# Kernel tuning notes

Measured on AMD Instinct MI355X. Metric: run time of the kernel, lower is better.

Reference implementation:

```python
import jax, jax.numpy as jnp
import numpy as np

N = 100000      # nodes
R = 8           # relations
E_DIM = 128     # embedding dim
N_EDGES = 1600000  # n * avg_degree(16)


def setup_inputs() -> dict:
    key = jax.random.key(0)
    k1, k2, k3, k4, k5 = jax.random.split(key, 5)
    x = jax.random.normal(k1, (N, E_DIM), dtype=jnp.float32)
    # xavier-ish scale for (r, e, e) relation weights
    weights = jax.random.normal(k2, (R, E_DIM, E_DIM), dtype=jnp.float32) * (1.0 / np.sqrt(E_DIM))
    edge_rel = jax.random.randint(k3, (N_EDGES,), 0, R, dtype=jnp.int32)
    edge_src = jax.random.randint(k4, (N_EDGES,), 0, N, dtype=jnp.int32)
    edge_dst = jax.random.randint(k5, (N_EDGES,), 0, N, dtype=jnp.int32)
    return dict(x=x, weights=weights, edge_rel=edge_rel, edge_src=edge_src, edge_dst=edge_dst)


def reference(x, weights, edge_rel, edge_src, edge_dst):
    n, e = x.shape
    r = weights.shape[0]
    # sparse adjacency row index: relation-block row = rel * n + dst  (shape rn)
    rows = edge_rel.astype(jnp.int32) * n + edge_dst.astype(jnp.int32)
    # row-normalized values: vals = 1 / row_degree (util.sum_sparse)
    deg = jax.ops.segment_sum(jnp.ones(rows.shape, dtype=x.dtype), rows, num_segments=r * n)
    vals = 1.0 / deg[rows]  # only evaluated at rows with >=1 edge
    # SpMM: h = graph @ x, viewed as (r, n, e)
    msgs = vals[:, None] * x[edge_src]                       # (E, e) gather
    h = jax.ops.segment_sum(msgs, rows, num_segments=r * n)  # (r*n, e) scatter-add
    h = h.reshape(r, n, e)
    # per-relation transform: (r, e_out, e_in) x (r, n, e_in) -> (n, r, e_out)
    h = jnp.einsum('rih,rnh->nri', weights, h)
    # SumUnify: relu(sum over relations)
    return jax.nn.relu(h.sum(axis=1))
```

## Files before the change

kernel.cpp:

```cpp
#include <hip/hip_runtime.h>
#include <hip/hip_bf16.h>

#define ED 128
#define RR 8
#define KTOT (RR * ED)
#define LDB 136

typedef __attribute__((ext_vector_type(8))) short short8;
typedef __attribute__((ext_vector_type(4))) float f32x4;
typedef __attribute__((ext_vector_type(4))) unsigned short u16x4;

#define RL(v, i) __builtin_amdgcn_readlane(v, i)

__device__ __forceinline__ unsigned short f2bf(float f){
  unsigned int u = __builtin_bit_cast(unsigned int, f);
  return (unsigned short)((u + 0x7fffu + ((u >> 16) & 1u)) >> 16);
}
__device__ __forceinline__ float bf2f(unsigned int lo){
  return __builtin_bit_cast(float, lo << 16);
}
__device__ __forceinline__ unsigned int packbf(float hi, float lo){
  return ((unsigned int)f2bf(hi) << 16) | f2bf(lo);
}

__global__ void cast_bf16_vec(const float* __restrict__ in, unsigned short* __restrict__ out, int n4){
  int stride = gridDim.x * blockDim.x;
  for (int i = blockIdx.x * blockDim.x + threadIdx.x; i < n4; i += stride){
    f32x4 v = __builtin_nontemporal_load((const f32x4*)(in + (size_t)i * 4));
    u16x4 o;
    o[0] = f2bf(v[0]); o[1] = f2bf(v[1]); o[2] = f2bf(v[2]); o[3] = f2bf(v[3]);
    *(u16x4*)(out + (size_t)i * 4) = o;
  }
}

__global__ void hist_rank(const int* __restrict__ rel, const int* __restrict__ dst,
                          int* __restrict__ rowcnt, int* __restrict__ rank, int E){
  int stride = gridDim.x * blockDim.x;
  for (int i = blockIdx.x * blockDim.x + threadIdx.x; i < E; i += stride)
    rank[i] = atomicAdd(&rowcnt[(dst[i] << 3) | rel[i]], 1);
}

__launch_bounds__(1024)
__global__ void scan_block_sum(const int* __restrict__ rowcnt, int* __restrict__ bsum, int m){
  __shared__ int lds[16];
  int t = threadIdx.x;
  int idx = blockIdx.x * 1024 + t;
  int v = (idx < m) ? rowcnt[idx] : 0;
#pragma unroll
  for (int o = 32; o > 0; o >>= 1) v += __shfl_down(v, o);
  if ((t & 63) == 0) lds[t >> 6] = v;
  __syncthreads();
  if (t == 0){
    int s = 0;
#pragma unroll
    for (int w = 0; w < 16; ++w) s += lds[w];
    bsum[blockIdx.x] = s;
  }
}

__launch_bounds__(1024)
__global__ void scan_bsum_par(const int* __restrict__ bsum, int* __restrict__ bscan,
                              int nb, int* __restrict__ total_out){
  __shared__ int wsum[16];
  int t = threadIdx.x, lane = t & 63, wid = t >> 6;
  int v = (t < nb) ? bsum[t] : 0;
  int incl = v;
#pragma unroll
  for (int o = 1; o < 64; o <<= 1){
    int u = __shfl_up(incl, o);
    if (lane >= o) incl += u;
  }
  if (lane == 63) wsum[wid] = incl;
  __syncthreads();
  int woff = 0;
  for (int w0 = 0; w0 < wid; ++w0) woff += wsum[w0];
  if (t < nb) bscan[t] = woff + incl - v;
  if (t == nb - 1) *total_out = woff + incl;
}

__launch_bounds__(1024)
__global__ void scan_final(const int* __restrict__ rowcnt, const int* __restrict__ bscan,
                           int* __restrict__ row_ptr, int m){
  __shared__ int wsum[16];
  int t = threadIdx.x, lane = t & 63, wid = t >> 6;
  int idx = blockIdx.x * 1024 + t;
  int v = (idx < m) ? rowcnt[idx] : 0;
  int incl = v;
#pragma unroll
  for (int o = 1; o < 64; o <<= 1){
    int u = __shfl_up(incl, o);
    if (lane >= o) incl += u;
  }
  if (lane == 63) wsum[wid] = incl;
  __syncthreads();
  int woff = bscan[blockIdx.x];
  for (int w0 = 0; w0 < wid; ++w0) woff += wsum[w0];
  if (idx < m) row_ptr[idx] = woff + incl - v;
}

__global__ void scatter_pos(const int* __restrict__ rel, const int* __restrict__ src,
                            const int* __restrict__ dst, const int* __restrict__ rank,
                            const int* __restrict__ row_ptr, int* __restrict__ payload, int E){
  int stride = gridDim.x * blockDim.x;
  for (int i = blockIdx.x * blockDim.x + threadIdx.x; i < E; i += stride){
    int key = (dst[i] << 3) | rel[i];
    payload[row_ptr[key] + rank[i]] = src[i];
  }
}

__launch_bounds__(256)
__global__ void row_agg(const unsigned short* __restrict__ xb,
                        const int* __restrict__ row_ptr8,
                        const int* __restrict__ payload,
                        unsigned short* __restrict__ h2, int n){
  int wv   = (blockIdx.x * 256 + threadIdx.x) >> 6;
  int lane = threadIdx.x & 63;
  int d    = wv >> 1;
  int half = wv & 1;
  if (d >= n) return;

  int p5 = 0;
  if (lane < 5) p5 = row_ptr8[(d << 3) + (half << 2) + lane];
  int b0  = RL(p5, 0);
  int o1  = RL(p5, 1) - b0;
  int o2  = RL(p5, 2) - b0;
  int o3  = RL(p5, 3) - b0;
  int cnt = RL(p5, 4) - b0;

  float ax0=0.f,ay0=0.f,ax1=0.f,ay1=0.f,ax2=0.f,ay2=0.f,ax3=0.f,ay3=0.f;

#define ROUTE(VV, IDX) { \
    float lo = bf2f((VV) & 0xffffu), hi = bf2f((VV) >> 16); \
    if ((IDX) < o1)      { ax0 += lo; ay0 += hi; } \
    else if ((IDX) < o2) { ax1 += lo; ay1 += hi; } \
    else if ((IDX) < o3) { ax2 += lo; ay2 += hi; } \
    else                 { ax3 += lo; ay3 += hi; } }

  if (cnt <= 64){
    int pl = payload[b0 + lane];
    int e = 0;
    for (; e + 4 <= cnt; e += 4){
      int s0 = RL(pl, e);
      int s1 = RL(pl, e + 1);
      int s2 = RL(pl, e + 2);
      int s3 = RL(pl, e + 3);
      unsigned int v0 = ((const unsigned int*)(xb + ((size_t)s0 << 7)))[lane];
      unsigned int v1 = ((const unsigned int*)(xb + ((size_t)s1 << 7)))[lane];
      unsigned int v2 = ((const unsigned int*)(xb + ((size_t)s2 << 7)))[lane];
      unsigned int v3 = ((const unsigned int*)(xb + ((size_t)s3 << 7)))[lane];
      ROUTE(v0, e)
      ROUTE(v1, e + 1)
      ROUTE(v2, e + 2)
      ROUTE(v3, e + 3)
    }
    for (; e < cnt; ++e){
      int s = RL(pl, e);
      unsigned int v = ((const unsigned int*)(xb + ((size_t)s << 7)))[lane];
      ROUTE(v, e)
    }
  } else {
    for (int e = 0; e < cnt; ++e){
      int s = __builtin_amdgcn_readfirstlane(payload[b0 + e]);
      unsigned int v = ((const unsigned int*)(xb + ((size_t)s << 7)))[lane];
      ROUTE(v, e)
    }
  }
#undef ROUTE

  int d0 = o1, d1 = o2 - o1, d2 = o3 - o2, d3 = cnt - o3;
  float s0f = d0 ? 1.f / (float)d0 : 0.f;
  float s1f = d1 ? 1.f / (float)d1 : 0.f;
  float s2f = d2 ? 1.f / (float)d2 : 0.f;
  float s3f = d3 ? 1.f / (float)d3 : 0.f;
  unsigned int* hp = (unsigned int*)h2 + ((size_t)d << 9) + (half << 8) + lane;
  __builtin_nontemporal_store(packbf(ay0 * s0f, ax0 * s0f), hp);
  __builtin_nontemporal_store(packbf(ay1 * s1f, ax1 * s1f), hp + 64);
  __builtin_nontemporal_store(packbf(ay2 * s2f, ax2 * s2f), hp + 128);
  __builtin_nontemporal_store(packbf(ay3 * s3f, ax3 * s3f), hp + 192);
}

__launch_bounds__(256)
__global__ void gemm_out(const unsigned short* __restrict__ h2,
                         const unsigned short* __restrict__ wbb,
                         float* __restrict__ out, int n){
  __shared__ __align__(16) unsigned short lds_a[128 * LDB];
  __shared__ __align__(16) unsigned short lds_b[128 * LDB];
  const int t = threadIdx.x;
  const int wave = t >> 6, lane = t & 63;
  const int wr = wave >> 1, wc = wave & 1;
  const int dbase = blockIdx.x * 128;
  const int frow = lane & 15, kb = lane >> 4;

  f32x4 acc[4][4];
#pragma unroll
  for (int rt = 0; rt < 4; ++rt)
#pragma unroll
    for (int jt = 0; jt < 4; ++jt)
      acc[rt][jt] = (f32x4){0.f, 0.f, 0.f, 0.f};

  for (int r = 0; r < RR; ++r){
    __syncthreads();
#pragma unroll
    for (int p = 0; p < 8; ++p){
      int q = p * 256 + t;
      int row = q >> 4, col = q & 15;
      int gr = dbase + row; if (gr >= n) gr = n - 1;
      short8 vv = __builtin_nontemporal_load(
          (const short8*)(h2 + (size_t)gr * KTOT + r * ED + col * 8));
      *(short8*)&lds_a[row * LDB + col * 8] = vv;
    }
    const unsigned short* wp = wbb + (size_t)r * ED * ED;
#pragma unroll
    for (int p = 0; p < 8; ++p){
      int q = p * 256 + t;
      int row = q >> 4, col = q & 15;
      *(short8*)&lds_b[row * LDB + col * 8] = *(const short8*)(wp + row * ED + col * 8);
    }
    __syncthreads();

    short8 a[4][4], b[4][4];
#pragma unroll
    for (int rt = 0; rt < 4; ++rt)
#pragma unroll
      for (int ks = 0; ks < 4; ++ks)
        a[rt][ks] = *(const short8*)&lds_a[(wr * 64 + rt * 16 + frow) * LDB + ks * 32 + kb * 8];
#pragma unroll
    for (int jt = 0; jt < 4; ++jt)
#pragma unroll
      for (int ks = 0; ks < 4; ++ks)
        b[jt][ks] = *(const short8*)&lds_b[(wc * 64 + jt * 16 + frow) * LDB + ks * 32 + kb * 8];
#pragma unroll
    for (int rt = 0; rt < 4; ++rt)
#pragma unroll
      for (int jt = 0; jt < 4; ++jt)
#pragma unroll
        for (int ks = 0; ks < 4; ++ks)
          acc[rt][jt] = __builtin_amdgcn_mfma_f32_16x16x32_bf16(a[rt][ks], b[jt][ks], acc[rt][jt], 0, 0, 0);
  }

  const int drow = (lane >> 4) * 4;
  const int dcol = lane & 15;
#pragma unroll
  for (int rt = 0; rt < 4; ++rt)
#pragma unroll
    for (int jt = 0; jt < 4; ++jt)
#pragma unroll
      for (int reg = 0; reg < 4; ++reg){
        int i = dbase + wr * 64 + rt * 16 + drow + reg;
        if (i < n)
          __builtin_nontemporal_store(fmaxf(acc[rt][jt][reg], 0.f),
                                      &out[(size_t)i * ED + wc * 64 + jt * 16 + dcol]);
      }
}

extern "C" void kernel_launch(void* const* d_in, const int* in_sizes, int n_in,
                              void* d_out, int out_size, void* d_ws, size_t ws_size,
                              hipStream_t stream){
  const float* x  = (const float*)d_in[0];
  const float* w  = (const float*)d_in[1];
  const int* erel = (const int*)d_in[2];
  const int* esrc = (const int*)d_in[3];
  const int* edst = (const int*)d_in[4];
  float* out = (float*)d_out;

  const int n = in_sizes[0] / ED;
  const int E = in_sizes[2];
  const int m = n * RR;
  const int NB = (m + 1023) / 1024;

  char* ws = (char*)d_ws;
  size_t off = 0;
  auto alloc = [&](size_t bytes) -> char* {
    char* p = ws + off;
    off += (bytes + 255) & ~(size_t)255;
    return p;
  };
  unsigned short* h2      = (unsigned short*)alloc((size_t)n * KTOT * 2);
  unsigned short* xb      = (unsigned short*)alloc((size_t)n * ED * 2);
  unsigned short* wbb     = (unsigned short*)alloc((size_t)RR * ED * ED * 2);
  int*            payload = (int*)alloc((size_t)E * 4);
  int*            row_ptr = (int*)alloc((size_t)(m + 1) * 4);
  int*            rowcnt  = (int*)alloc((size_t)m * 4);
  int*            rank    = (int*)alloc((size_t)E * 4);
  int*            bsum    = (int*)alloc((size_t)NB * 4);
  int*            bscan   = (int*)alloc((size_t)NB * 4);
  if (off > ws_size || NB > 1024) return;

  (void)hipMemsetAsync(rowcnt, 0, (size_t)m * 4, stream);

  cast_bf16_vec<<<2048, 256, 0, stream>>>(x, xb, n * ED / 4);
  cast_bf16_vec<<<128, 256, 0, stream>>>(w, wbb, RR * ED * ED / 4);
  hist_rank    <<<2048, 256, 0, stream>>>(erel, edst, rowcnt, rank, E);
  scan_block_sum<<<NB, 1024, 0, stream>>>(rowcnt, bsum, m);
  scan_bsum_par<<<1, 1024, 0, stream>>>(bsum, bscan, NB, row_ptr + m);
  scan_final   <<<NB, 1024, 0, stream>>>(rowcnt, bscan, row_ptr, m);
  scatter_pos  <<<2048, 256, 0, stream>>>(erel, esrc, edst, rank, row_ptr, payload, E);
  row_agg      <<<(2 * n + 3) / 4, 256, 0, stream>>>(xb, row_ptr, payload, h2, n);
  gemm_out     <<<(n + 127) / 128, 256, 0, stream>>>(h2, wbb, out, n);
}
```

Before: 293.0 us.

## Aggregate all relations per node in one wave; prefetch next relation tiles in GEMM

```diff
diff --git a/kernel.cpp b/kernel.cpp
--- a/kernel.cpp
+++ b/kernel.cpp
@@ -113,45 +113,63 @@
                         const int* __restrict__ row_ptr8,
                         const int* __restrict__ payload,
                         unsigned short* __restrict__ h2, int n){
-  int wv   = (blockIdx.x * 256 + threadIdx.x) >> 6;
+  int d    = (blockIdx.x * 256 + threadIdx.x) >> 6;
   int lane = threadIdx.x & 63;
-  int d    = wv >> 1;
-  int half = wv & 1;
   if (d >= n) return;
 
-  int p5 = 0;
-  if (lane < 5) p5 = row_ptr8[(d << 3) + (half << 2) + lane];
-  int b0  = RL(p5, 0);
-  int o1  = RL(p5, 1) - b0;
-  int o2  = RL(p5, 2) - b0;
-  int o3  = RL(p5, 3) - b0;
-  int cnt = RL(p5, 4) - b0;
+  int p9 = 0;
+  if (lane < 9) p9 = row_ptr8[(d << 3) + lane];
+  int b0  = RL(p9, 0);
+  int o1  = RL(p9, 1) - b0;
+  int o2  = RL(p9, 2) - b0;
+  int o3  = RL(p9, 3) - b0;
+  int o4  = RL(p9, 4) - b0;
+  int o5  = RL(p9, 5) - b0;
+  int o6  = RL(p9, 6) - b0;
+  int o7  = RL(p9, 7) - b0;
+  int cnt = RL(p9, 8) - b0;
 
   float ax0=0.f,ay0=0.f,ax1=0.f,ay1=0.f,ax2=0.f,ay2=0.f,ax3=0.f,ay3=0.f;
+  float ax4=0.f,ay4=0.f,ax5=0.f,ay5=0.f,ax6=0.f,ay6=0.f,ax7=0.f,ay7=0.f;
 
 #define ROUTE(VV, IDX) { \
     float lo = bf2f((VV) & 0xffffu), hi = bf2f((VV) >> 16); \
-    if ((IDX) < o1)      { ax0 += lo; ay0 += hi; } \
-    else if ((IDX) < o2) { ax1 += lo; ay1 += hi; } \
-    else if ((IDX) < o3) { ax2 += lo; ay2 += hi; } \
-    else                 { ax3 += lo; ay3 += hi; } }
+    if ((IDX) < o4){ \
+      if ((IDX) < o2){ if ((IDX) < o1){ ax0+=lo; ay0+=hi; } else { ax1+=lo; ay1+=hi; } } \
+      else           { if ((IDX) < o3){ ax2+=lo; ay2+=hi; } else { ax3+=lo; ay3+=hi; } } \
+    } else { \
+      if ((IDX) < o6){ if ((IDX) < o5){ ax4+=lo; ay4+=hi; } else { ax5+=lo; ay5+=hi; } } \
+      else           { if ((IDX) < o7){ ax6+=lo; ay6+=hi; } else { ax7+=lo; ay7+=hi; } } \
+    } }
 
   if (cnt <= 64){
     int pl = payload[b0 + lane];
     int e = 0;
-    for (; e + 4 <= cnt; e += 4){
+    for (; e + 8 <= cnt; e += 8){
       int s0 = RL(pl, e);
       int s1 = RL(pl, e + 1);
       int s2 = RL(pl, e + 2);
       int s3 = RL(pl, e + 3);
+      int s4 = RL(pl, e + 4);
+      int s5 = RL(pl, e + 5);
+      int s6 = RL(pl, e + 6);
+      int s7 = RL(pl, e + 7);
       unsigned int v0 = ((const unsigned int*)(xb + ((size_t)s0 << 7)))[lane];
       unsigned int v1 = ((const unsigned int*)(xb + ((size_t)s1 << 7)))[lane];
       unsigned int v2 = ((const unsigned int*)(xb + ((size_t)s2 << 7)))[lane];
       unsigned int v3 = ((const unsigned int*)(xb + ((size_t)s3 << 7)))[lane];
+      unsigned int v4 = ((const unsigned int*)(xb + ((size_t)s4 << 7)))[lane];
+      unsigned int v5 = ((const unsigned int*)(xb + ((size_t)s5 << 7)))[lane];
+      unsigned int v6 = ((const unsigned int*)(xb + ((size_t)s6 << 7)))[lane];
+      unsigned int v7 = ((const unsigned int*)(xb + ((size_t)s7 << 7)))[lane];
       ROUTE(v0, e)
       ROUTE(v1, e + 1)
       ROUTE(v2, e + 2)
       ROUTE(v3, e + 3)
+      ROUTE(v4, e + 4)
+      ROUTE(v5, e + 5)
+      ROUTE(v6, e + 6)
+      ROUTE(v7, e + 7)
     }
     for (; e < cnt; ++e){
       int s = RL(pl, e);
@@ -167,16 +185,18 @@
   }
 #undef ROUTE
 
-  int d0 = o1, d1 = o2 - o1, d2 = o3 - o2, d3 = cnt - o3;
-  float s0f = d0 ? 1.f / (float)d0 : 0.f;
-  float s1f = d1 ? 1.f / (float)d1 : 0.f;
-  float s2f = d2 ? 1.f / (float)d2 : 0.f;
-  float s3f = d3 ? 1.f / (float)d3 : 0.f;
-  unsigned int* hp = (unsigned int*)h2 + ((size_t)d << 9) + (half << 8) + lane;
-  __builtin_nontemporal_store(packbf(ay0 * s0f, ax0 * s0f), hp);
-  __builtin_nontemporal_store(packbf(ay1 * s1f, ax1 * s1f), hp + 64);
-  __builtin_nontemporal_store(packbf(ay2 * s2f, ax2 * s2f), hp + 128);
-  __builtin_nontemporal_store(packbf(ay3 * s3f, ax3 * s3f), hp + 192);
+  int c0 = o1, c1 = o2 - o1, c2 = o3 - o2, c3 = o4 - o3;
+  int c4 = o5 - o4, c5 = o6 - o5, c6 = o7 - o6, c7 = cnt - o7;
+  unsigned int* hp = (unsigned int*)h2 + ((size_t)d << 9) + lane;
+  float sc;
+  sc = c0 ? 1.f / (float)c0 : 0.f; __builtin_nontemporal_store(packbf(ay0*sc, ax0*sc), hp);
+  sc = c1 ? 1.f / (float)c1 : 0.f; __builtin_nontemporal_store(packbf(ay1*sc, ax1*sc), hp + 64);
+  sc = c2 ? 1.f / (float)c2 : 0.f; __builtin_nontemporal_store(packbf(ay2*sc, ax2*sc), hp + 128);
+  sc = c3 ? 1.f / (float)c3 : 0.f; __builtin_nontemporal_store(packbf(ay3*sc, ax3*sc), hp + 192);
+  sc = c4 ? 1.f / (float)c4 : 0.f; __builtin_nontemporal_store(packbf(ay4*sc, ax4*sc), hp + 256);
+  sc = c5 ? 1.f / (float)c5 : 0.f; __builtin_nontemporal_store(packbf(ay5*sc, ax5*sc), hp + 320);
+  sc = c6 ? 1.f / (float)c6 : 0.f; __builtin_nontemporal_store(packbf(ay6*sc, ax6*sc), hp + 384);
+  sc = c7 ? 1.f / (float)c7 : 0.f; __builtin_nontemporal_store(packbf(ay7*sc, ax7*sc), hp + 448);
 }
 
 __launch_bounds__(256)
@@ -198,25 +218,38 @@
     for (int jt = 0; jt < 4; ++jt)
       acc[rt][jt] = (f32x4){0.f, 0.f, 0.f, 0.f};
 
+  short8 pa[8], pb[8];
+#pragma unroll
+  for (int p = 0; p < 8; ++p){
+    int q = p * 256 + t;
+    int row = q >> 4, col = q & 15;
+    int gr = dbase + row; if (gr >= n) gr = n - 1;
+    pa[p] = __builtin_nontemporal_load((const short8*)(h2 + (size_t)gr * KTOT + col * 8));
+    pb[p] = *(const short8*)(wbb + row * ED + col * 8);
+  }
+
   for (int r = 0; r < RR; ++r){
     __syncthreads();
 #pragma unroll
     for (int p = 0; p < 8; ++p){
       int q = p * 256 + t;
       int row = q >> 4, col = q & 15;
-      int gr = dbase + row; if (gr >= n) gr = n - 1;
-      short8 vv = __builtin_nontemporal_load(
-          (const short8*)(h2 + (size_t)gr * KTOT + r * ED + col * 8));
-      *(short8*)&lds_a[row * LDB + col * 8] = vv;
-    }
-    const unsigned short* wp = wbb + (size_t)r * ED * ED;
-#pragma unroll
-    for (int p = 0; p < 8; ++p){
-      int q = p * 256 + t;
-      int row = q >> 4, col = q & 15;
-      *(short8*)&lds_b[row * LDB + col * 8] = *(const short8*)(wp + row * ED + col * 8);
+      *(short8*)&lds_a[row * LDB + col * 8] = pa[p];
+      *(short8*)&lds_b[row * LDB + col * 8] = pb[p];
     }
     __syncthreads();
+
+    if (r + 1 < RR){
+#pragma unroll
+      for (int p = 0; p < 8; ++p){
+        int q = p * 256 + t;
+        int row = q >> 4, col = q & 15;
+        int gr = dbase + row; if (gr >= n) gr = n - 1;
+        pa[p] = __builtin_nontemporal_load(
+            (const short8*)(h2 + (size_t)gr * KTOT + (r + 1) * ED + col * 8));
+        pb[p] = *(const short8*)(wbb + (size_t)(r + 1) * ED * ED + row * ED + col * 8);
+      }
+    }
 
     short8 a[4][4], b[4][4];
 #pragma unroll
@@ -295,6 +328,6 @@
   scan_bsum_par<<<1, 1024, 0, stream>>>(bsum, bscan, NB, row_ptr + m);
   scan_final   <<<NB, 1024, 0, stream>>>(rowcnt, bscan, row_ptr, m);
   scatter_pos  <<<2048, 256, 0, stream>>>(erel, esrc, edst, rank, row_ptr, payload, E);
-  row_agg      <<<(2 * n + 3) / 4, 256, 0, stream>>>(xb, row_ptr, payload, h2, n);
+  row_agg      <<<(n + 3) / 4, 256, 0, stream>>>(xb, row_ptr, payload, h2, n);
   gemm_out     <<<(n + 127) / 128, 256, 0, stream>>>(h2, wbb, out, n);
 }
```

Result: faster. 284.4 us (-3.0%).
